# Kernel tuning notes

Measured on AMD Instinct MI355X. Metric: run time of the kernel, lower is better.

The kernel has to match this reference:

```python
import jax, jax.numpy as jnp
import numpy as np

N = 100000   # nodes
E = 1600000  # edges
IN = 32
HID = 64
OUT = 1

def setup_inputs() -> dict:
    key = jax.random.key(0)
    ks = jax.random.split(key, 16)
    x = jax.random.normal(ks[0], (N, IN), jnp.float32)
    edge_index = jax.random.randint(ks[1], (2, E), 0, N, dtype=jnp.int32)
    def lin(k, fi, fo):
        return jax.random.normal(k, (fi, fo), jnp.float32) / np.sqrt(fi)
    # SAGEConv params per layer: Wn/bn for aggregated neighbors (lin_l), Wr for root (lin_r, no bias)
    Wn0 = lin(ks[2], IN, HID);  bn0 = jnp.zeros((HID,), jnp.float32); Wr0 = lin(ks[3], IN, HID)
    Wn1 = lin(ks[4], HID, HID); bn1 = jnp.zeros((HID,), jnp.float32); Wr1 = lin(ks[5], HID, HID)
    Wn2 = lin(ks[6], HID, HID); bn2 = jnp.zeros((HID,), jnp.float32); Wr2 = lin(ks[7], HID, HID)
    # predictor MLP
    Wp1 = lin(ks[8], HID, HID); bp1 = jnp.zeros((HID,), jnp.float32)
    Wp2 = lin(ks[9], HID, OUT); bp2 = jnp.zeros((OUT,), jnp.float32)
    return dict(x=x, edge_index=edge_index,
                Wn0=Wn0, bn0=bn0, Wr0=Wr0,
                Wn1=Wn1, bn1=bn1, Wr1=Wr1,
                Wn2=Wn2, bn2=bn2, Wr2=Wr2,
                Wp1=Wp1, bp1=bp1, Wp2=Wp2, bp2=bp2)

def reference(x, edge_index, Wn0, bn0, Wr0, Wn1, bn1, Wr1, Wn2, bn2, Wr2, Wp1, bp1, Wp2, bp2):
    src, dst = edge_index[0], edge_index[1]
    n = x.shape[0]
    # mean-aggregation normalization (nodes with no in-edges get 0, as in PyG)
    cnt = jax.ops.segment_sum(jnp.ones(src.shape, x.dtype), dst, num_segments=n)
    inv = jnp.where(cnt > 0, 1.0 / jnp.maximum(cnt, 1.0), 0.0)[:, None]

    def sage(h, Wn, bn, Wr):
        agg = jax.ops.segment_sum(h[src], dst, num_segments=n) * inv  # [N, d]
        return agg @ Wn + bn + h @ Wr

    h = jax.nn.relu(sage(x, Wn0, bn0, Wr0))
    h = jax.nn.relu(sage(h, Wn1, bn1, Wr1))
    h = sage(h, Wn2, bn2, Wr2)  # no activation after last GNN layer
    h = jax.nn.relu(h @ Wp1 + bp1)
    return jax.nn.sigmoid(h @ Wp2 + bp2)
```

## Files before the change

kernel.cpp:

```cpp
#include <hip/hip_runtime.h>
#include <math.h>

#define NN 100000
#define EE 1600000
#define HID 64
#define BKT 391
#define SLAB 5504
#define SLAB_IT ((SLAB + 255) / 256)
#define CHUNK 4096
#define NWG ((EE + CHUNK - 1) / CHUNK)
#define TB (NN / 16)

typedef _Float16 f16;
typedef _Float16 f16x2 __attribute__((ext_vector_type(2)));

__device__ __forceinline__ f16x2 u2h(unsigned u) { return __builtin_bit_cast(f16x2, u); }
__device__ __forceinline__ unsigned h2u(f16x2 h) { return __builtin_bit_cast(unsigned, h); }

#if defined(__has_builtin) && __has_builtin(__builtin_amdgcn_fdot2)
__device__ __forceinline__ float dot2(f16x2 a, f16x2 b, float c) {
    return __builtin_amdgcn_fdot2(a, b, c, false);
}
#else
__device__ __forceinline__ float dot2(f16x2 a, f16x2 b, float c) {
    c = fmaf((float)a.x, (float)b.x, c);
    return fmaf((float)a.y, (float)b.y, c);
}
#endif


#if defined(__has_builtin)
#if __has_builtin(__builtin_amdgcn_cvt_pk_f32_fp8) && __has_builtin(__builtin_amdgcn_cvt_pk_fp8_f32)
#define HW_FP8 1
#endif
#endif

#ifndef HW_FP8
__device__ __forceinline__ float dec_e4m3(unsigned b) {
    unsigned s = b >> 7, e = (b >> 3) & 0xF, m = b & 7;
    float v;
    if (e == 0) v = (float)m * 0.001953125f;
    else v = (1.f + (float)m * 0.125f) * exp2f((float)((int)e - 7));
    return s ? -v : v;
}
__device__ __forceinline__ unsigned char enc_e4m3(float x) {
    unsigned s = (__builtin_bit_cast(unsigned, x) >> 31) << 7;
    float a = fabsf(x);
    if (!(a < 464.f)) return (unsigned char)(s | 0x7E);
    int e; float m = frexpf(a, &e);
    int E = e - 1;
    unsigned bits;
    if (E < -6) {
        int n = (int)rintf(a * 512.f);
        bits = (n > 7) ? 0x08u : (unsigned)n;
    } else {
        int n = (int)rintf((2.f * m - 1.f) * 8.f);
        if (n == 8) { n = 0; E += 1; }
        if (E > 8) return (unsigned char)(s | 0x7E);
        bits = ((unsigned)(E + 7) << 3) | (unsigned)n;
    }
    return (unsigned char)(s | bits);
}
#endif

__device__ __forceinline__ void acc_fp8(unsigned v, float& a0, float& a1,
                                        float& a2, float& a3) {
#ifdef HW_FP8
    auto lo = __builtin_amdgcn_cvt_pk_f32_fp8((int)v, false);
    auto hi = __builtin_amdgcn_cvt_pk_f32_fp8((int)v, true);
    a0 += lo[0]; a1 += lo[1]; a2 += hi[0]; a3 += hi[1];
#else
    a0 += dec_e4m3(v & 0xFFu);         a1 += dec_e4m3((v >> 8) & 0xFFu);
    a2 += dec_e4m3((v >> 16) & 0xFFu); a3 += dec_e4m3(v >> 24);
#endif
}

__device__ __forceinline__ unsigned char enc_fp8(float x) {
#ifdef HW_FP8
    return (unsigned char)(__builtin_amdgcn_cvt_pk_fp8_f32(x, x, 0, false) & 0xFF);
#else
    return enc_e4m3(x);
#endif
}


__global__ void mt_kernel(const int* __restrict__ src, const int* __restrict__ dst,
                          int* __restrict__ bfill, unsigned* __restrict__ pairs,
                          const float* __restrict__ h,
                          const float* __restrict__ Wn, const float* __restrict__ bn,
                          const float* __restrict__ Wr,
                          unsigned char* __restrict__ hn8, f16* __restrict__ hrb,
                          const float* __restrict__ Wn1, const float* __restrict__ Wr1,
                          const float* __restrict__ Wn2, const float* __restrict__ Wr2,
                          const float* __restrict__ Wp1, unsigned* __restrict__ w16) {
    __shared__ int lc[BKT];
    __shared__ int lbase[BKT];
    int t = threadIdx.x;

    if (blockIdx.x < NWG) {
        for (int b = t; b < BKT; b += 256) lc[b] = 0;
        __syncthreads();
        int base = blockIdx.x * CHUNK;
        int myd[CHUNK / 256];
        int myr[CHUNK / 256];
#pragma unroll
        for (int j = 0; j < CHUNK / 256; ++j) {
            int i = base + j * 256 + t;
            myd[j] = (i < EE) ? dst[i] : -1;
            myr[j] = (myd[j] >= 0) ? atomicAdd(&lc[myd[j] >> 8], 1) : 0;
        }
        __syncthreads();
        for (int b = t; b < BKT; b += 256) {
            int c = lc[b];
            if (c) {
                int ofs = atomicAdd(&bfill[b], c);
                if (ofs + c > SLAB) ofs = SLAB - c;
                lbase[b] = b * SLAB + ofs;
            }
        }
        __syncthreads();
#pragma unroll
        for (int j = 0; j < CHUNK / 256; ++j) {
            int i = base + j * 256 + t;
            if (myd[j] >= 0) {
                int b = myd[j] >> 8;
                pairs[lbase[b] + myr[j]] = (unsigned)src[i] | ((unsigned)(myd[j] & 255) << 24);
            }
        }
        return;
    }

    int bb = blockIdx.x - NWG;

    if (bb < 40) {
        int id = bb * 256 + t;
        int mat = id >> 11;
        int p = (id >> 6) & 31;
        int j = id & 63;
        const float* W = (mat == 0) ? Wn1 : (mat == 1) ? Wr1 :
                         (mat == 2) ? Wn2 : (mat == 3) ? Wr2 : Wp1;
        f16x2 v;
        v.x = (f16)W[(2 * p) * HID + j];
        v.y = (f16)W[(2 * p + 1) * HID + j];
        w16[id] = h2u(v);
    }

    int lane = t & 63;
    int wid = (bb * 256 + t) >> 6;
    int m0 = __builtin_amdgcn_readfirstlane(wid << 2);
    const float* h0 = h + (size_t)m0 * 32;

    float an0 = 0.f, an1 = 0.f, an2 = 0.f, an3 = 0.f;
    float ar0 = 0.f, ar1 = 0.f, ar2 = 0.f, ar3 = 0.f;
#pragma unroll
    for (int k = 0; k < 32; ++k) {
        float wn = Wn[k * HID + lane];
        float wr = Wr[k * HID + lane];
        float hk0 = h0[k], hk1 = h0[32 + k], hk2 = h0[64 + k], hk3 = h0[96 + k];
        an0 = fmaf(hk0, wn, an0); ar0 = fmaf(hk0, wr, ar0);
        an1 = fmaf(hk1, wn, an1); ar1 = fmaf(hk1, wr, ar1);
        an2 = fmaf(hk2, wn, an2); ar2 = fmaf(hk2, wr, ar2);
        an3 = fmaf(hk3, wn, an3); ar3 = fmaf(hk3, wr, ar3);
    }
    float b = bn[lane];
    size_t o8 = (size_t)m0 * HID + lane;
    hn8[o8] = enc_fp8(an0);
    hn8[o8 + HID] = enc_fp8(an1);
    hn8[o8 + 2 * HID] = enc_fp8(an2);
    hn8[o8 + 3 * HID] = enc_fp8(an3);
    size_t o = (size_t)m0 * HID + lane;
    hrb[o] = (f16)(ar0 + b); hrb[o + HID] = (f16)(ar1 + b);
    hrb[o + 2 * HID] = (f16)(ar2 + b); hrb[o + 3 * HID] = (f16)(ar3 + b);
}


__global__ void build_kernel(const unsigned* __restrict__ pairs,
                             const int* __restrict__ bfill,
                             int* __restrict__ rs, int* __restrict__ re,
                             float* __restrict__ inv, int* __restrict__ col) {
    __shared__ int ncnt[256];
    __shared__ int nexcl[256];
    int b = blockIdx.x;
    int t = threadIdx.x;
    int s0 = b * SLAB;
    int ce = bfill[b]; if (ce > SLAB) ce = SLAB;
    ncnt[t] = 0;
    __syncthreads();
    unsigned mypk[SLAB_IT];
    int myr[SLAB_IT];
#pragma unroll
    for (int j = 0; j < SLAB_IT; ++j) {
        int e = j * 256 + t;
        if (e < ce) {
            unsigned pk = pairs[s0 + e];
            mypk[j] = pk;
            myr[j] = atomicAdd(&ncnt[pk >> 24], 1);
        }
    }
    __syncthreads();
    int c = ncnt[t];
    nexcl[t] = c;
    __syncthreads();
    for (int off = 1; off < 256; off <<= 1) {
        int u = (t >= off) ? nexcl[t - off] : 0;
        __syncthreads();
        nexcl[t] += u;
        __syncthreads();
    }
    int excl = nexcl[t] - c;
    int node = (b << 8) + t;
    if (node < NN) {
        rs[node] = s0 + excl;
        re[node] = s0 + excl + c;
        inv[node] = (c > 0) ? (1.0f / (float)c) : 0.0f;
    }
    __syncthreads();
    ncnt[t] = excl;
    __syncthreads();
#pragma unroll
    for (int j = 0; j < SLAB_IT; ++j) {
        int e = j * 256 + t;
        if (e < ce) {
            unsigned pk = mypk[j];
            col[s0 + ncnt[pk >> 24] + myr[j]] = (int)(pk & 0xFFFFFFu);
        }
    }
}


__device__ __forceinline__ void qgather8(const unsigned* __restrict__ rp,
                                         const int* __restrict__ col,
                                         int e, int en, int fl,
                                         float& a0, float& a1, float& a2, float& a3) {
    while (e + 8 <= en) {
        int c0 = col[e],     c1 = col[e + 1], c2 = col[e + 2], c3 = col[e + 3];
        int c4 = col[e + 4], c5 = col[e + 5], c6 = col[e + 6], c7 = col[e + 7];
        unsigned v0 = rp[(size_t)c0 * 16 + fl];
        unsigned v1 = rp[(size_t)c1 * 16 + fl];
        unsigned v2 = rp[(size_t)c2 * 16 + fl];
        unsigned v3 = rp[(size_t)c3 * 16 + fl];
        unsigned v4 = rp[(size_t)c4 * 16 + fl];
        unsigned v5 = rp[(size_t)c5 * 16 + fl];
        unsigned v6 = rp[(size_t)c6 * 16 + fl];
        unsigned v7 = rp[(size_t)c7 * 16 + fl];
        acc_fp8(v0, a0, a1, a2, a3);
        acc_fp8(v1, a0, a1, a2, a3);
        acc_fp8(v2, a0, a1, a2, a3);
        acc_fp8(v3, a0, a1, a2, a3);
        acc_fp8(v4, a0, a1, a2, a3);
        acc_fp8(v5, a0, a1, a2, a3);
        acc_fp8(v6, a0, a1, a2, a3);
        acc_fp8(v7, a0, a1, a2, a3);
        e += 8;
    }
    if (e + 4 <= en) {
        int c0 = col[e], c1 = col[e + 1], c2 = col[e + 2], c3 = col[e + 3];
        unsigned v0 = rp[(size_t)c0 * 16 + fl];
        unsigned v1 = rp[(size_t)c1 * 16 + fl];
        unsigned v2 = rp[(size_t)c2 * 16 + fl];
        unsigned v3 = rp[(size_t)c3 * 16 + fl];
        acc_fp8(v0, a0, a1, a2, a3);
        acc_fp8(v1, a0, a1, a2, a3);
        acc_fp8(v2, a0, a1, a2, a3);
        acc_fp8(v3, a0, a1, a2, a3);
        e += 4;
    }
    while (e < en) {
        unsigned v = rp[(size_t)col[e] * 16 + fl];
        acc_fp8(v, a0, a1, a2, a3);
        ++e;
    }
}


__global__ void gt_kernel(const unsigned char* __restrict__ An8,
                          const int* __restrict__ rs, const int* __restrict__ re,
                          const int* __restrict__ col, const float* __restrict__ inv,
                          f16* C,
                          const unsigned* __restrict__ Wn16, const float* __restrict__ bn,
                          const unsigned* __restrict__ Wr16,
                          unsigned char* __restrict__ Aout8) {
    int lane = threadIdx.x & 63;
    int wid = (blockIdx.x * blockDim.x + threadIdx.x) >> 6;
    int m0 = wid << 2;
    int m = m0 + (lane >> 4);
    int fl = lane & 15;

    float a0 = 0.f, a1 = 0.f, a2 = 0.f, a3 = 0.f;
    qgather8((const unsigned*)An8, col, rs[m], re[m], fl, a0, a1, a2, a3);

    float iv = inv[m];
    uint2 cur = ((const uint2*)C)[(size_t)m * 16 + fl];
    f16x2 q0 = u2h(cur.x), q1 = u2h(cur.y);
    f16x2 hA, hB;
    hA.x = (f16)fmaxf(fmaf(a0, iv, (float)q0.x), 0.f);
    hA.y = (f16)fmaxf(fmaf(a1, iv, (float)q0.y), 0.f);
    hB.x = (f16)fmaxf(fmaf(a2, iv, (float)q1.x), 0.f);
    hB.y = (f16)fmaxf(fmaf(a3, iv, (float)q1.y), 0.f);
    unsigned hx = h2u(hA), hy = h2u(hB);

    float an[4] = {0.f, 0.f, 0.f, 0.f};
    float ar[4] = {0.f, 0.f, 0.f, 0.f};
#pragma unroll
    for (int kk = 0; kk < 16; ++kk) {
        f16x2 wnA = u2h(Wn16[(2 * kk) * HID + lane]);
        f16x2 wnB = u2h(Wn16[(2 * kk + 1) * HID + lane]);
        f16x2 wrA = u2h(Wr16[(2 * kk) * HID + lane]);
        f16x2 wrB = u2h(Wr16[(2 * kk + 1) * HID + lane]);
#pragma unroll
        for (int n = 0; n < 4; ++n) {
            f16x2 px = u2h(__shfl(hx, (n << 4) + kk));
            f16x2 py = u2h(__shfl(hy, (n << 4) + kk));
            an[n] = dot2(px, wnA, an[n]);
            an[n] = dot2(py, wnB, an[n]);
            ar[n] = dot2(px, wrA, ar[n]);
            ar[n] = dot2(py, wrB, ar[n]);
        }
    }
    float b = bn[lane];
    size_t o8 = (size_t)m0 * HID + lane;
    size_t o = (size_t)m0 * HID + lane;
#pragma unroll
    for (int n = 0; n < 4; ++n) {
        Aout8[o8 + n * HID] = enc_fp8(an[n]);
        C[o + n * HID] = (f16)(ar[n] + b);
    }
}


__global__ void gh_kernel(const unsigned char* __restrict__ An8,
                          const int* __restrict__ rs, const int* __restrict__ re,
                          const int* __restrict__ col, const float* __restrict__ inv,
                          const f16* __restrict__ C,
                          const unsigned* __restrict__ Wp116, const float* __restrict__ bp1,
                          const float* __restrict__ Wp2, const float* __restrict__ bp2,
                          float* __restrict__ out) {
    int lane = threadIdx.x & 63;
    int wid = (blockIdx.x * blockDim.x + threadIdx.x) >> 6;
    int m0 = wid << 2;
    int m = m0 + (lane >> 4);
    int fl = lane & 15;

    float a0 = 0.f, a1 = 0.f, a2 = 0.f, a3 = 0.f;
    qgather8((const unsigned*)An8, col, rs[m], re[m], fl, a0, a1, a2, a3);

    float iv = inv[m];
    uint2 cur = ((const uint2*)C)[(size_t)m * 16 + fl];
    f16x2 q0 = u2h(cur.x), q1 = u2h(cur.y);
    f16x2 hA, hB;
    hA.x = (f16)fmaf(a0, iv, (float)q0.x);
    hA.y = (f16)fmaf(a1, iv, (float)q0.y);
    hB.x = (f16)fmaf(a2, iv, (float)q1.x);
    hB.y = (f16)fmaf(a3, iv, (float)q1.y);
    unsigned hx = h2u(hA), hy = h2u(hB);

    float tn[4] = {0.f, 0.f, 0.f, 0.f};
#pragma unroll
    for (int kk = 0; kk < 16; ++kk) {
        f16x2 wA = u2h(Wp116[(2 * kk) * HID + lane]);
        f16x2 wB = u2h(Wp116[(2 * kk + 1) * HID + lane]);
#pragma unroll
        for (int n = 0; n < 4; ++n) {
            f16x2 px = u2h(__shfl(hx, (n << 4) + kk));
            f16x2 py = u2h(__shfl(hy, (n << 4) + kk));
            tn[n] = dot2(px, wA, tn[n]);
            tn[n] = dot2(py, wB, tn[n]);
        }
    }
    float b = bp1[lane], w2v = Wp2[lane];
    float r0 = fmaxf(tn[0] + b, 0.f) * w2v;
    float r1 = fmaxf(tn[1] + b, 0.f) * w2v;
    float r2 = fmaxf(tn[2] + b, 0.f) * w2v;
    float r3 = fmaxf(tn[3] + b, 0.f) * w2v;
#pragma unroll
    for (int off = 32; off > 0; off >>= 1) {
        r0 += __shfl_xor(r0, off);
        r1 += __shfl_xor(r1, off);
        r2 += __shfl_xor(r2, off);
        r3 += __shfl_xor(r3, off);
    }
    if (lane == 0) {
        float bb = bp2[0];
        out[m0]     = 1.f / (1.f + expf(-(r0 + bb)));
        out[m0 + 1] = 1.f / (1.f + expf(-(r1 + bb)));
        out[m0 + 2] = 1.f / (1.f + expf(-(r2 + bb)));
        out[m0 + 3] = 1.f / (1.f + expf(-(r3 + bb)));
    }
}

extern "C" void kernel_launch(void* const* d_in, const int* in_sizes, int n_in,
                              void* d_out, int out_size, void* d_ws, size_t ws_size,
                              hipStream_t stream) {
    const float* x   = (const float*)d_in[0];
    const int* eidx  = (const int*)d_in[1];
    const float* Wn0 = (const float*)d_in[2];
    const float* bn0 = (const float*)d_in[3];
    const float* Wr0 = (const float*)d_in[4];
    const float* Wn1 = (const float*)d_in[5];
    const float* bn1 = (const float*)d_in[6];
    const float* Wr1 = (const float*)d_in[7];
    const float* Wn2 = (const float*)d_in[8];
    const float* bn2 = (const float*)d_in[9];
    const float* Wr2 = (const float*)d_in[10];
    const float* Wp1 = (const float*)d_in[11];
    const float* bp1 = (const float*)d_in[12];
    const float* Wp2 = (const float*)d_in[13];
    const float* bp2 = (const float*)d_in[14];
    float* out = (float*)d_out;

    const int* src = eidx;
    const int* dst = eidx + EE;

    char* w = (char*)d_ws;
    size_t off = 0;
    auto carve = [&](size_t bytes) -> void* {
        void* p = w + off;
        off = (off + bytes + 255) & ~(size_t)255;
        return p;
    };
    int*   rsA    = (int*)carve((size_t)NN * 4);
    int*   reA    = (int*)carve((size_t)NN * 4);
    float* inv    = (float*)carve((size_t)NN * 4);
    int*   col    = (int*)carve((size_t)BKT * SLAB * 4);
    int*   bfill  = (int*)carve((size_t)BKT * 4);
    unsigned* w16 = (unsigned*)carve((size_t)5 * 2048 * 4);
    unsigned char* A0 = (unsigned char*)carve((size_t)NN * HID);
    unsigned char* A1 = (unsigned char*)carve((size_t)NN * HID);
    f16*   C      = (f16*)carve((size_t)NN * HID * 2);
    unsigned* pairs = (unsigned*)carve((size_t)BKT * SLAB * 4);
    (void)ws_size;

    unsigned* Wn1_16 = w16;
    unsigned* Wr1_16 = w16 + 2048;
    unsigned* Wn2_16 = w16 + 4096;
    unsigned* Wr2_16 = w16 + 6144;
    unsigned* Wp1_16 = w16 + 8192;

    hipMemsetAsync(bfill, 0, (size_t)BKT * 4, stream);

    mt_kernel<<<NWG + TB, 256, 0, stream>>>(src, dst, bfill, pairs,
                                            x, Wn0, bn0, Wr0, A0, C,
                                            Wn1, Wr1, Wn2, Wr2, Wp1, w16);
    build_kernel<<<BKT, 256, 0, stream>>>(pairs, bfill, rsA, reA, inv, col);

    gt_kernel<<<TB, 256, 0, stream>>>(A0, rsA, reA, col, inv, C, Wn1_16, bn1, Wr1_16, A1);
    gt_kernel<<<TB, 256, 0, stream>>>(A1, rsA, reA, col, inv, C, Wn2_16, bn2, Wr2_16, A0);
    gh_kernel<<<TB, 256, 0, stream>>>(A0, rsA, reA, col, inv, C, Wp1_16, bp1, Wp2, bp2, out);
}
```

Measured before the change: 274.6 us.

## Pad CSR rows to multiples of four and stage hidden rows in LDS

The CSR build now pads each node's neighbor list to a multiple of four, filling the padding with a dummy node index that points at a zeroed extra feature row. This lets the gather loop fetch column indices with 16-byte int4 loads instead of scalar loads. The per-row matvec now reads the hidden vector from LDS as uint4 instead of broadcasting it with cross-lane shuffles, which cuts shuffle traffic. In exchange it adds padding that consumes slab capacity, needs clamping at slab boundaries, and adds extra memsets for the dummy rows.

```diff
diff --git a/kernel.cpp b/kernel.cpp
--- a/kernel.cpp
+++ b/kernel.cpp
@@ -199,7 +199,8 @@
     }
     __syncthreads();
     int c = ncnt[t];
-    nexcl[t] = c;
+    int c4 = (c + 3) & ~3;
+    nexcl[t] = c4;
     __syncthreads();
     for (int off = 1; off < 256; off <<= 1) {
         int u = (t >= off) ? nexcl[t - off] : 0;
@@ -207,11 +208,13 @@
         nexcl[t] += u;
         __syncthreads();
     }
-    int excl = nexcl[t] - c;
+    int excl = nexcl[t] - c4;
     int node = (b << 8) + t;
     if (node < NN) {
-        rs[node] = s0 + excl;
-        re[node] = s0 + excl + c;
+        int start = s0 + excl; if (start > s0 + SLAB) start = s0 + SLAB;
+        int end = start + c;   if (end > s0 + SLAB) end = s0 + SLAB;
+        rs[node] = start;
+        re[node] = end;
         inv[node] = (c > 0) ? (1.0f / (float)c) : 0.0f;
     }
     __syncthreads();
@@ -222,27 +225,32 @@
         int e = j * 256 + t;
         if (e < ce) {
             unsigned pk = mypk[j];
-            col[s0 + ncnt[pk >> 24] + myr[j]] = (int)(pk & 0xFFFFFFu);
-        }
+            int idx = s0 + ncnt[pk >> 24] + myr[j];
+            if (idx < s0 + SLAB) col[idx] = (int)(pk & 0xFFFFFFu);
+        }
+    }
+    for (int k = c; k < c4; ++k) {
+        int idx = s0 + excl + k;
+        if (idx < s0 + SLAB) col[idx] = NN;
     }
 }
 
 
 __device__ __forceinline__ void qgather8(const unsigned* __restrict__ rp,
                                          const int* __restrict__ col,
-                                         int e, int en, int fl,
+                                         int e, int en, int en4, int fl,
                                          float& a0, float& a1, float& a2, float& a3) {
-    while (e + 8 <= en) {
-        int c0 = col[e],     c1 = col[e + 1], c2 = col[e + 2], c3 = col[e + 3];
-        int c4 = col[e + 4], c5 = col[e + 5], c6 = col[e + 6], c7 = col[e + 7];
-        unsigned v0 = rp[(size_t)c0 * 16 + fl];
-        unsigned v1 = rp[(size_t)c1 * 16 + fl];
-        unsigned v2 = rp[(size_t)c2 * 16 + fl];
-        unsigned v3 = rp[(size_t)c3 * 16 + fl];
-        unsigned v4 = rp[(size_t)c4 * 16 + fl];
-        unsigned v5 = rp[(size_t)c5 * 16 + fl];
-        unsigned v6 = rp[(size_t)c6 * 16 + fl];
-        unsigned v7 = rp[(size_t)c7 * 16 + fl];
+    while (e + 8 <= en4) {
+        int4 ca = *(const int4*)(col + e);
+        int4 cb = *(const int4*)(col + e + 4);
+        unsigned v0 = rp[(size_t)ca.x * 16 + fl];
+        unsigned v1 = rp[(size_t)ca.y * 16 + fl];
+        unsigned v2 = rp[(size_t)ca.z * 16 + fl];
+        unsigned v3 = rp[(size_t)ca.w * 16 + fl];
+        unsigned v4 = rp[(size_t)cb.x * 16 + fl];
+        unsigned v5 = rp[(size_t)cb.y * 16 + fl];
+        unsigned v6 = rp[(size_t)cb.z * 16 + fl];
+        unsigned v7 = rp[(size_t)cb.w * 16 + fl];
         acc_fp8(v0, a0, a1, a2, a3);
         acc_fp8(v1, a0, a1, a2, a3);
         acc_fp8(v2, a0, a1, a2, a3);
@@ -253,12 +261,12 @@
         acc_fp8(v7, a0, a1, a2, a3);
         e += 8;
     }
-    if (e + 4 <= en) {
-        int c0 = col[e], c1 = col[e + 1], c2 = col[e + 2], c3 = col[e + 3];
-        unsigned v0 = rp[(size_t)c0 * 16 + fl];
-        unsigned v1 = rp[(size_t)c1 * 16 + fl];
-        unsigned v2 = rp[(size_t)c2 * 16 + fl];
-        unsigned v3 = rp[(size_t)c3 * 16 + fl];
+    if (e + 4 <= en4) {
+        int4 ca = *(const int4*)(col + e);
+        unsigned v0 = rp[(size_t)ca.x * 16 + fl];
+        unsigned v1 = rp[(size_t)ca.y * 16 + fl];
+        unsigned v2 = rp[(size_t)ca.z * 16 + fl];
+        unsigned v3 = rp[(size_t)ca.w * 16 + fl];
         acc_fp8(v0, a0, a1, a2, a3);
         acc_fp8(v1, a0, a1, a2, a3);
         acc_fp8(v2, a0, a1, a2, a3);
@@ -280,14 +288,22 @@
                           const unsigned* __restrict__ Wn16, const float* __restrict__ bn,
                           const unsigned* __restrict__ Wr16,
                           unsigned char* __restrict__ Aout8) {
-    int lane = threadIdx.x & 63;
-    int wid = (blockIdx.x * blockDim.x + threadIdx.x) >> 6;
+    __shared__ uint4 hsh[128];
+    int t = threadIdx.x;
+    int lane = t & 63;
+    int wv = t >> 6;
+    int wid = (blockIdx.x * blockDim.x + t) >> 6;
     int m0 = wid << 2;
     int m = m0 + (lane >> 4);
     int fl = lane & 15;
 
+    int e = rs[m], en = re[m];
+    int en4 = e + ((en - e + 3) & ~3);
+    int bnd = ((m >> 8) + 1) * SLAB;
+    if (en4 > bnd) en4 = bnd;
+
     float a0 = 0.f, a1 = 0.f, a2 = 0.f, a3 = 0.f;
-    qgather8((const unsigned*)An8, col, rs[m], re[m], fl, a0, a1, a2, a3);
+    qgather8((const unsigned*)An8, col, e, en, en4, fl, a0, a1, a2, a3);
 
     float iv = inv[m];
     uint2 cur = ((const uint2*)C)[(size_t)m * 16 + fl];
@@ -297,24 +313,33 @@
     hA.y = (f16)fmaxf(fmaf(a1, iv, (float)q0.y), 0.f);
     hB.x = (f16)fmaxf(fmaf(a2, iv, (float)q1.x), 0.f);
     hB.y = (f16)fmaxf(fmaf(a3, iv, (float)q1.y), 0.f);
-    unsigned hx = h2u(hA), hy = h2u(hB);
+
+    uint2 hv; hv.x = h2u(hA); hv.y = h2u(hB);
+    ((uint2*)hsh)[wv * 64 + (lane >> 4) * 16 + fl] = hv;
 
     float an[4] = {0.f, 0.f, 0.f, 0.f};
     float ar[4] = {0.f, 0.f, 0.f, 0.f};
 #pragma unroll
-    for (int kk = 0; kk < 16; ++kk) {
-        f16x2 wnA = u2h(Wn16[(2 * kk) * HID + lane]);
-        f16x2 wnB = u2h(Wn16[(2 * kk + 1) * HID + lane]);
-        f16x2 wrA = u2h(Wr16[(2 * kk) * HID + lane]);
-        f16x2 wrB = u2h(Wr16[(2 * kk + 1) * HID + lane]);
+    for (int j = 0; j < 8; ++j) {
+        f16x2 wn0 = u2h(Wn16[(4 * j) * HID + lane]);
+        f16x2 wn1 = u2h(Wn16[(4 * j + 1) * HID + lane]);
+        f16x2 wn2 = u2h(Wn16[(4 * j + 2) * HID + lane]);
+        f16x2 wn3 = u2h(Wn16[(4 * j + 3) * HID + lane]);
+        f16x2 wr0 = u2h(Wr16[(4 * j) * HID + lane]);
+        f16x2 wr1 = u2h(Wr16[(4 * j + 1) * HID + lane]);
+        f16x2 wr2 = u2h(Wr16[(4 * j + 2) * HID + lane]);
+        f16x2 wr3 = u2h(Wr16[(4 * j + 3) * HID + lane]);
 #pragma unroll
         for (int n = 0; n < 4; ++n) {
-            f16x2 px = u2h(__shfl(hx, (n << 4) + kk));
-            f16x2 py = u2h(__shfl(hy, (n << 4) + kk));
-            an[n] = dot2(px, wnA, an[n]);
-            an[n] = dot2(py, wnB, an[n]);
-            ar[n] = dot2(px, wrA, ar[n]);
-            ar[n] = dot2(py, wrB, ar[n]);
+            uint4 d = hsh[wv * 32 + n * 8 + j];
+            an[n] = dot2(u2h(d.x), wn0, an[n]);
+            an[n] = dot2(u2h(d.y), wn1, an[n]);
+            an[n] = dot2(u2h(d.z), wn2, an[n]);
+            an[n] = dot2(u2h(d.w), wn3, an[n]);
+            ar[n] = dot2(u2h(d.x), wr0, ar[n]);
+            ar[n] = dot2(u2h(d.y), wr1, ar[n]);
+            ar[n] = dot2(u2h(d.z), wr2, ar[n]);
+            ar[n] = dot2(u2h(d.w), wr3, ar[n]);
         }
     }
     float b = bn[lane];
@@ -335,14 +360,22 @@
                           const unsigned* __restrict__ Wp116, const float* __restrict__ bp1,
                           const float* __restrict__ Wp2, const float* __restrict__ bp2,
                           float* __restrict__ out) {
-    int lane = threadIdx.x & 63;
-    int wid = (blockIdx.x * blockDim.x + threadIdx.x) >> 6;
+    __shared__ uint4 hsh[128];
+    int t = threadIdx.x;
+    int lane = t & 63;
+    int wv = t >> 6;
+    int wid = (blockIdx.x * blockDim.x + t) >> 6;
     int m0 = wid << 2;
     int m = m0 + (lane >> 4);
     int fl = lane & 15;
 
+    int e = rs[m], en = re[m];
+    int en4 = e + ((en - e + 3) & ~3);
+    int bnd = ((m >> 8) + 1) * SLAB;
+    if (en4 > bnd) en4 = bnd;
+
     float a0 = 0.f, a1 = 0.f, a2 = 0.f, a3 = 0.f;
-    qgather8((const unsigned*)An8, col, rs[m], re[m], fl, a0, a1, a2, a3);
+    qgather8((const unsigned*)An8, col, e, en, en4, fl, a0, a1, a2, a3);
 
     float iv = inv[m];
     uint2 cur = ((const uint2*)C)[(size_t)m * 16 + fl];
@@ -352,19 +385,24 @@
     hA.y = (f16)fmaf(a1, iv, (float)q0.y);
     hB.x = (f16)fmaf(a2, iv, (float)q1.x);
     hB.y = (f16)fmaf(a3, iv, (float)q1.y);
-    unsigned hx = h2u(hA), hy = h2u(hB);
+
+    uint2 hv; hv.x = h2u(hA); hv.y = h2u(hB);
+    ((uint2*)hsh)[wv * 64 + (lane >> 4) * 16 + fl] = hv;
 
     float tn[4] = {0.f, 0.f, 0.f, 0.f};
 #pragma unroll
-    for (int kk = 0; kk < 16; ++kk) {
-        f16x2 wA = u2h(Wp116[(2 * kk) * HID + lane]);
-        f16x2 wB = u2h(Wp116[(2 * kk + 1) * HID + lane]);
+    for (int j = 0; j < 8; ++j) {
+        f16x2 wp0 = u2h(Wp116[(4 * j) * HID + lane]);
+        f16x2 wp1 = u2h(Wp116[(4 * j + 1) * HID + lane]);
+        f16x2 wp2 = u2h(Wp116[(4 * j + 2) * HID + lane]);
+        f16x2 wp3 = u2h(Wp116[(4 * j + 3) * HID + lane]);
 #pragma unroll
         for (int n = 0; n < 4; ++n) {
-            f16x2 px = u2h(__shfl(hx, (n << 4) + kk));
-            f16x2 py = u2h(__shfl(hy, (n << 4) + kk));
-            tn[n] = dot2(px, wA, tn[n]);
-            tn[n] = dot2(py, wB, tn[n]);
+            uint4 d = hsh[wv * 32 + n * 8 + j];
+            tn[n] = dot2(u2h(d.x), wp0, tn[n]);
+            tn[n] = dot2(u2h(d.y), wp1, tn[n]);
+            tn[n] = dot2(u2h(d.z), wp2, tn[n]);
+            tn[n] = dot2(u2h(d.w), wp3, tn[n]);
         }
     }
     float b = bp1[lane], w2v = Wp2[lane];
@@ -424,8 +462,8 @@
     int*   col    = (int*)carve((size_t)BKT * SLAB * 4);
     int*   bfill  = (int*)carve((size_t)BKT * 4);
     unsigned* w16 = (unsigned*)carve((size_t)5 * 2048 * 4);
-    unsigned char* A0 = (unsigned char*)carve((size_t)NN * HID);
-    unsigned char* A1 = (unsigned char*)carve((size_t)NN * HID);
+    unsigned char* A0 = (unsigned char*)carve((size_t)(NN + 1) * HID);
+    unsigned char* A1 = (unsigned char*)carve((size_t)(NN + 1) * HID);
     f16*   C      = (f16*)carve((size_t)NN * HID * 2);
     unsigned* pairs = (unsigned*)carve((size_t)BKT * SLAB * 4);
     (void)ws_size;
@@ -437,6 +475,8 @@
     unsigned* Wp1_16 = w16 + 8192;
 
     hipMemsetAsync(bfill, 0, (size_t)BKT * 4, stream);
+    hipMemsetAsync(A0 + (size_t)NN * HID, 0, HID, stream);
+    hipMemsetAsync(A1 + (size_t)NN * HID, 0, HID, stream);
 
     mt_kernel<<<NWG + TB, 256, 0, stream>>>(src, dst, bfill, pairs,
                                             x, Wn0, bn0, Wr0, A0, C,
```

Measured after the change: 244.2 us. 11.1% less time.
